# Optimization experiments

Measured on AMD Instinct MI355X. Metric: run time of the kernel, lower is better.

Reference implementation:

```python
import jax, jax.numpy as jnp
import numpy as np


def _block_triu_mask(seq_len, rows_per_block, cols_per_block, dtype=jnp.float32):
    # Block upper-triangular mask: block (i, j) is ones iff j >= i.
    tri = jnp.triu(jnp.ones((seq_len, seq_len), dtype=dtype))
    return jnp.kron(tri, jnp.ones((rows_per_block, cols_per_block), dtype=dtype))


def setup_inputs() -> dict:
    key = jax.random.key(0)
    k_x, k_w1, k_w2 = jax.random.split(key, 3)
    seq_len, input_dim, hidden_dim, output_dim = 64, 64, 128, 64
    batch = 256
    x = jax.random.normal(k_x, (batch, seq_len, input_dim), dtype=jnp.float32)
    # kaiming_uniform_(a=sqrt(5)) on [fan_in, fan_out] tensor -> bound = 1/sqrt(fan_in)
    fan1 = seq_len * input_dim
    W1 = jax.random.uniform(k_w1, (seq_len * input_dim, seq_len * hidden_dim),
                            minval=-1.0, maxval=1.0, dtype=jnp.float32) / np.sqrt(fan1)
    b1 = jnp.zeros((seq_len * hidden_dim,), dtype=jnp.float32)
    fan2 = seq_len * hidden_dim
    W2 = jax.random.uniform(k_w2, (seq_len * hidden_dim, seq_len * output_dim),
                            minval=-1.0, maxval=1.0, dtype=jnp.float32) / np.sqrt(fan2)
    b2 = jnp.zeros((seq_len * output_dim,), dtype=jnp.float32)
    return {"x": x, "W1": W1, "b1": b1, "W2": W2, "b2": b2, "seq_len": seq_len}


def reference(x, W1, b1, W2, b2, seq_len):
    batch = x.shape[0]
    input_dim = x.shape[2]
    hidden_dim = W1.shape[1] // seq_len
    output_dim = W2.shape[1] // seq_len
    mask1 = _block_triu_mask(seq_len, input_dim, hidden_dim, W1.dtype)
    mask2 = _block_triu_mask(seq_len, hidden_dim, output_dim, W2.dtype)
    h = x.reshape(batch, seq_len * input_dim)
    h = jnp.matmul(h, W1 * mask1) + b1           # [B, S*H]
    h = jax.nn.relu(h)
    h = jnp.matmul(h, W2 * mask2) + b2           # [B, S*O]
    return h.reshape(batch, seq_len, output_dim)
```

## Files before the change

kernel.cpp:

```cpp
#include <hip/hip_runtime.h>

typedef short bf16x8 __attribute__((ext_vector_type(8)));
typedef float f32x4 __attribute__((ext_vector_type(4)));

__device__ __forceinline__ unsigned short f2bf(float f) {
  unsigned x = __float_as_uint(f);
  return (unsigned short)((x + 0x7fffu + ((x >> 16) & 1u)) >> 16);
}


__device__ __forceinline__ int chunkbase1(int p) {
  const int a = p >> 1, b = p & 1;
  const int al = a >> 3, be = a & 7;
  const int C8 = 4 * al * (al + 1) + be * (al + 1);
  return 2 * C8 + b * ((a + 8) >> 3);
}
__device__ __forceinline__ int chunkbase2(int p) {
  const int al = p >> 2, be = p & 3;
  return 2 * al * (al + 1) + be * (al + 1);
}

__global__ __launch_bounds__(256)
void pack_x(const float* __restrict__ x, unsigned short* __restrict__ img) {
  const int i = (blockIdx.x * 256 + threadIdx.x) * 8;
  const int m = i >> 12, k = i & 4095;
  float q[8];
  *(float4*)(q)     = *(const float4*)(x + i);
  *(float4*)(q + 4) = *(const float4*)(x + i + 4);
  union { unsigned short u[8]; int4 v; } t;
#pragma unroll
  for (int j = 0; j < 8; ++j) t.u[j] = f2bf(q[j]);
  const size_t o = (size_t)(k >> 6) * 16384 + m * 64 + ((k & 63) ^ ((m & 7) << 3));
  *(int4*)(img + o) = t.v;
}

template<int PSH, int KSH, int MODE>
__global__ __launch_bounds__(256, 2)
void gemm_sk(const unsigned short* __restrict__ Aimg,
             const float* __restrict__ W,
             float* __restrict__ part, int N) {
  __shared__ unsigned short Ws[64 * 72];

  const int p = (int)gridDim.x - 1 - (int)blockIdx.x;
  const int c = blockIdx.y;
  const int nt = ((p >> PSH) + 1) << KSH;
  const int i0 = c * 8;
  if (i0 >= nt) return;
  const int i1 = (i0 + 8 < nt) ? i0 + 8 : nt;
  const int base = (MODE == 1) ? chunkbase1(p) : chunkbase2(p);
  float* po = part + (size_t)(base + c) * 16384;

  const int tid = threadIdx.x, lane = tid & 63, wave = tid >> 6;
  const int l15 = lane & 15, quad = lane >> 4;

  const int l16 = tid & 15, rg = tid >> 4;
  const float* wbase = W + (size_t)p * 64 + l16 * 4;

  int aoff[4][2];
#pragma unroll
  for (int mi = 0; mi < 4; ++mi) {
    const int m = wave * 64 + mi * 16 + l15;
#pragma unroll
    for (int h = 0; h < 2; ++h) {
      const int k8 = h * 32 + quad * 8;
      aoff[mi][h] = m * 64 + (k8 ^ ((m & 7) << 3));
    }
  }

  float4 wr[4];
  bf16x8 afA[4][2], afB[4][2];

  auto loadW = [&](int kt) {
#pragma unroll
    for (int j = 0; j < 4; ++j)
      wr[j] = *(const float4*)(wbase + (size_t)(kt * 64 + rg + j * 16) * N);
  };
  auto loadA = [&](bf16x8 (&af)[4][2], int kt) {
    const unsigned short* at = Aimg + (size_t)kt * 16384;
#pragma unroll
    for (int mi = 0; mi < 4; ++mi)
#pragma unroll
      for (int h = 0; h < 2; ++h)
        af[mi][h] = *(const bf16x8*)(at + aoff[mi][h]);
  };
  auto storeW = [&]() {
#pragma unroll
    for (int j = 0; j < 4; ++j) {
      const int r = rg + j * 16;
      const float* f = (const float*)&wr[j];
#pragma unroll
      for (int i = 0; i < 4; ++i) {
        const int cc = l16 * 4 + i;
        Ws[cc * 72 + (r ^ (((cc >> 3) & 7) << 3))] = f2bf(f[i]);
      }
    }
  };

  f32x4 acc[4][4];
#pragma unroll
  for (int mi = 0; mi < 4; ++mi)
#pragma unroll
    for (int ni = 0; ni < 4; ++ni)
      acc[mi][ni] = (f32x4){0.f, 0.f, 0.f, 0.f};

  auto STEP = [&](bf16x8 (&cur)[4][2], bf16x8 (&nxt)[4][2], int it) {
    __syncthreads();
    storeW();
    if (it + 1 < i1) { loadW(it + 1); loadA(nxt, it + 1); }
    __syncthreads();
#pragma unroll
    for (int h = 0; h < 2; ++h) {
      const int kk = h * 32;
      bf16x8 bfr[4];
#pragma unroll
      for (int ni = 0; ni < 4; ++ni) {
        const int n = ni * 16 + l15;
        bfr[ni] = *(const bf16x8*)(
            &Ws[n * 72 + ((kk + quad * 8) ^ (((n >> 3) & 7) << 3))]);
      }
#pragma unroll
      for (int mi = 0; mi < 4; ++mi)
#pragma unroll
        for (int ni = 0; ni < 4; ++ni)
          acc[mi][ni] = __builtin_amdgcn_mfma_f32_16x16x32_bf16(
              cur[mi][h], bfr[ni], acc[mi][ni], 0, 0, 0);
    }
  };

  loadW(i0);
  loadA(afA, i0);
  int it = i0;
  while (true) {
    STEP(afA, afB, it); if (++it >= i1) break;
    STEP(afB, afA, it); if (++it >= i1) break;
  }

  float* ps = po + wave * 4096 + lane;
#pragma unroll
  for (int mi = 0; mi < 4; ++mi)
#pragma unroll
    for (int ni = 0; ni < 4; ++ni)
#pragma unroll
      for (int r = 0; r < 4; ++r)
        ps[mi * 1024 + ni * 256 + r * 64] = acc[mi][ni][r];
}

__global__ __launch_bounds__(256)
void reduce1(const float* __restrict__ P, const float* __restrict__ b1,
             unsigned short* __restrict__ img) {
  const int g = blockIdx.x * 256 + threadIdx.x;
  const int p = g >> 12;
  const int s = (g & 4095) * 4;
  const int nc = ((p >> 1) + 8) >> 3;
  const float* ps = P + (size_t)chunkbase1(p) * 16384 + s;
  f32x4 a = *(const f32x4*)ps;
  for (int ci = 1; ci < nc; ++ci)
    a += *(const f32x4*)(ps + (size_t)ci * 16384);
  const int lane = s & 63, r = (s >> 6) & 3, ni = (s >> 8) & 3;
  const int mi = (s >> 10) & 3, wv = (s >> 12) & 3;
  const int m  = wv * 64 + mi * 16 + (lane >> 4) * 4 + r;
  const int nl = ni * 16 + (lane & 15);
  a += *(const f32x4*)(b1 + p * 64 + nl);
  union { unsigned short u[4]; int2 v; } t;
#pragma unroll
  for (int j = 0; j < 4; ++j) t.u[j] = f2bf(fmaxf(a[j], 0.f));
  *(int2*)(img + (size_t)p * 16384 + m * 64 + (nl ^ ((m & 7) << 3))) = t.v;
}

__global__ __launch_bounds__(256)
void reduce2(const float* __restrict__ P, const float* __restrict__ b2,
             float* __restrict__ out) {
  const int g = blockIdx.x * 256 + threadIdx.x;
  const int p = g >> 12;
  const int s = (g & 4095) * 4;
  const int nc = (p + 4) >> 2;
  const float* ps = P + (size_t)chunkbase2(p) * 16384 + s;
  f32x4 a = *(const f32x4*)ps;
  for (int ci = 1; ci < nc; ++ci)
    a += *(const f32x4*)(ps + (size_t)ci * 16384);
  const int lane = s & 63, r = (s >> 6) & 3, ni = (s >> 8) & 3;
  const int mi = (s >> 10) & 3, wv = (s >> 12) & 3;
  const int m  = wv * 64 + mi * 16 + (lane >> 4) * 4 + r;
  const int nl = ni * 16 + (lane & 15);
  a += *(const f32x4*)(b2 + p * 64 + nl);
  *(f32x4*)(out + (size_t)m * 4096 + p * 64 + nl) = a;
}

extern "C" void kernel_launch(void* const* d_in, const int* in_sizes, int n_in,
                              void* d_out, int out_size, void* d_ws, size_t ws_size,
                              hipStream_t stream) {
  const float* x  = (const float*)d_in[0];
  const float* W1 = (const float*)d_in[1];
  const float* b1 = (const float*)d_in[2];
  const float* W2 = (const float*)d_in[3];
  const float* b2 = (const float*)d_in[4];

  char* ws = (char*)d_ws;
  unsigned short* Ximg = (unsigned short*)ws;
  unsigned short* Himg = (unsigned short*)(ws + 2097152);
  float*          P    = (float*)(ws + 6291456);
  float* out = (float*)d_out;

  pack_x<<<dim3(512), 256, 0, stream>>>(x, Ximg);

  gemm_sk<1, 0, 1><<<dim3(128, 8), 256, 0, stream>>>(Ximg, W1, P, 8192);

  reduce1<<<dim3(2048), 256, 0, stream>>>(P, b1, Himg);

  gemm_sk<0, 1, 2><<<dim3(64, 16), 256, 0, stream>>>(Himg, W2, P, 4096);

  reduce2<<<dim3(1024), 256, 0, stream>>>(P, b2, out);
}
```

Measured before the change: 338.5 us.

## Widen GEMM tiles to 128x256 with LDS-staged A and fused x packing

Replaces the 256x64-tile split-K GEMM with a 512-thread kernel that computes 128x256 tiles, stages both A and W through shared memory, and converts x from fp32 to bf16 inside the GEMM so the separate pack kernel disappears. Panels now span 256 output columns, with per-element masking applied at the partial diagonal block. The goal is more reuse of each W load across output rows and fewer launches. The cost is that some masked-out W is still loaded, a larger LDS footprint, and a new partial-sum layout that the reductions must follow.

```diff
diff --git a/kernel.cpp b/kernel.cpp
--- a/kernel.cpp
+++ b/kernel.cpp
@@ -7,92 +7,96 @@
   unsigned x = __float_as_uint(f);
   return (unsigned short)((x + 0x7fffu + ((x >> 16) & 1u)) >> 16);
 }
-
-
-__device__ __forceinline__ int chunkbase1(int p) {
-  const int a = p >> 1, b = p & 1;
-  const int al = a >> 3, be = a & 7;
-  const int C8 = 4 * al * (al + 1) + be * (al + 1);
-  return 2 * C8 + b * ((a + 8) >> 3);
-}
-__device__ __forceinline__ int chunkbase2(int p) {
-  const int al = p >> 2, be = p & 3;
-  return 2 * al * (al + 1) + be * (al + 1);
-}
-
-__global__ __launch_bounds__(256)
-void pack_x(const float* __restrict__ x, unsigned short* __restrict__ img) {
-  const int i = (blockIdx.x * 256 + threadIdx.x) * 8;
-  const int m = i >> 12, k = i & 4095;
-  float q[8];
-  *(float4*)(q)     = *(const float4*)(x + i);
-  *(float4*)(q + 4) = *(const float4*)(x + i + 4);
-  union { unsigned short u[8]; int4 v; } t;
-#pragma unroll
-  for (int j = 0; j < 8; ++j) t.u[j] = f2bf(q[j]);
-  const size_t o = (size_t)(k >> 6) * 16384 + m * 64 + ((k & 63) ^ ((m & 7) << 3));
-  *(int4*)(img + o) = t.v;
-}
-
-template<int PSH, int KSH, int MODE>
-__global__ __launch_bounds__(256, 2)
-void gemm_sk(const unsigned short* __restrict__ Aimg,
-             const float* __restrict__ W,
-             float* __restrict__ part, int N) {
-  __shared__ unsigned short Ws[64 * 72];
-
-  const int p = (int)gridDim.x - 1 - (int)blockIdx.x;
-  const int c = blockIdx.y;
-  const int nt = ((p >> PSH) + 1) << KSH;
+__device__ __forceinline__ unsigned b32pair(float a, float b) {
+  return (unsigned)f2bf(a) | ((unsigned)f2bf(b) << 16);
+}
+
+template<int MODE>
+__global__ __launch_bounds__(512, 2)
+void gemm_w(const void* __restrict__ Av, const float* __restrict__ W,
+            float* __restrict__ P) {
+  constexpr int NPAN = (MODE == 1) ? 32 : 16;
+  constexpr int K    = (MODE == 1) ? 4096 : 8192;
+  constexpr int N    = (MODE == 1) ? 8192 : 4096;
+
+  __shared__ unsigned short Ws[256 * 64];
+  __shared__ unsigned short Xs[128 * 64];
+
+  const int p  = NPAN - 1 - (int)blockIdx.z;
+  const int mt = blockIdx.y;
+  const int c  = blockIdx.x;
+  const int nt = (MODE == 1) ? (2 * p + 2) : (8 * p + 8);
   const int i0 = c * 8;
   if (i0 >= nt) return;
-  const int i1 = (i0 + 8 < nt) ? i0 + 8 : nt;
-  const int base = (MODE == 1) ? chunkbase1(p) : chunkbase2(p);
-  float* po = part + (size_t)(base + c) * 16384;
-
-  const int tid = threadIdx.x, lane = tid & 63, wave = tid >> 6;
+  const int i1 = (i0 + 8 < nt) ? (i0 + 8) : nt;
+  const int a4 = p >> 2;
+  const int base = (MODE == 1) ? ((a4 + 1) * (2 * a4 + (p & 3)))
+                               : (p * (p + 1) / 2);
+  float* po = P + ((size_t)(base + c) * 2 + mt) * 32768;
+
+  const int tid = threadIdx.x;
+  const int lane = tid & 63, w = tid >> 6;
   const int l15 = lane & 15, quad = lane >> 4;
-
-  const int l16 = tid & 15, rg = tid >> 4;
-  const float* wbase = W + (size_t)p * 64 + l16 * 4;
-
-  int aoff[4][2];
-#pragma unroll
-  for (int mi = 0; mi < 4; ++mi) {
-    const int m = wave * 64 + mi * 16 + l15;
-#pragma unroll
-    for (int h = 0; h < 2; ++h) {
-      const int k8 = h * 32 + quad * 8;
-      aoff[mi][h] = m * 64 + (k8 ^ ((m & 7) << 3));
-    }
-  }
-
-  float4 wr[4];
-  bf16x8 afA[4][2], afB[4][2];
+  const int wm = w >> 2, wn = w & 3;
+  const int swa = (l15 & 7) << 3;
+
+  const int wr0 = (tid >> 4) * 2;
+  const int wc0 = (tid & 15) * 16;
+  const float* wsrc = W + (size_t)p * 256 + wc0;
+
+  const int ar = tid >> 2;
+  const int ak0 = (tid & 3) * 16;
+
+  float4 wv[8];
+  float4 av[4];
+  int4   ab[2];
 
   auto loadW = [&](int kt) {
-#pragma unroll
-    for (int j = 0; j < 4; ++j)
-      wr[j] = *(const float4*)(wbase + (size_t)(kt * 64 + rg + j * 16) * N);
-  };
-  auto loadA = [&](bf16x8 (&af)[4][2], int kt) {
-    const unsigned short* at = Aimg + (size_t)kt * 16384;
-#pragma unroll
-    for (int mi = 0; mi < 4; ++mi)
-#pragma unroll
-      for (int h = 0; h < 2; ++h)
-        af[mi][h] = *(const bf16x8*)(at + aoff[mi][h]);
-  };
-  auto storeW = [&]() {
-#pragma unroll
-    for (int j = 0; j < 4; ++j) {
-      const int r = rg + j * 16;
-      const float* f = (const float*)&wr[j];
-#pragma unroll
-      for (int i = 0; i < 4; ++i) {
-        const int cc = l16 * 4 + i;
-        Ws[cc * 72 + (r ^ (((cc >> 3) & 7) << 3))] = f2bf(f[i]);
+    const float* r0p = wsrc + (size_t)(kt * 64 + wr0) * N;
+#pragma unroll
+    for (int j = 0; j < 4; ++j) wv[j] = *(const float4*)(r0p + j * 4);
+#pragma unroll
+    for (int j = 0; j < 4; ++j) wv[4 + j] = *(const float4*)(r0p + N + j * 4);
+  };
+  auto storeW = [&](int kt) {
+    const int kg = kt * 64 + wr0;
+    const float* f = (const float*)wv;
+#pragma unroll
+    for (int i = 0; i < 16; ++i) {
+      const int cc = wc0 + i;
+      const int lk = (MODE == 1) ? ((2 * p + (cc >> 7) + 1) * 64)
+                                 : ((4 * p + (cc >> 6) + 1) * 128);
+      const float v0 = (kg < lk) ? f[i] : 0.f;
+      const float v1 = (kg + 1 < lk) ? f[16 + i] : 0.f;
+      const int sw = ((cc ^ (cc >> 3)) & 7) << 3;
+      *(unsigned*)&Ws[cc * 64 + (wr0 ^ sw)] = b32pair(v0, v1);
+    }
+  };
+  auto loadA = [&](int kt) {
+    if constexpr (MODE == 1) {
+      const float* ap = (const float*)Av + (size_t)(mt * 128 + ar) * K
+                        + kt * 64 + ak0;
+#pragma unroll
+      for (int j = 0; j < 4; ++j) av[j] = *(const float4*)(ap + j * 4);
+    } else {
+      const unsigned short* ap = (const unsigned short*)Av
+          + (size_t)(mt * 128 + ar) * K + kt * 64 + ak0;
+      ab[0] = *(const int4*)ap;
+      ab[1] = *(const int4*)(ap + 8);
+    }
+  };
+  auto storeA = [&]() {
+    if constexpr (MODE == 1) {
+      const float* f = (const float*)av;
+      const int sa = (ar & 7) << 3;
+#pragma unroll
+      for (int j = 0; j < 8; ++j) {
+        const int kl = ak0 + 2 * j;
+        *(unsigned*)&Xs[ar * 64 + (kl ^ sa)] = b32pair(f[2 * j], f[2 * j + 1]);
       }
+    } else {
+      *(int4*)&Xs[ar * 64 + ak0]     = ab[0];
+      *(int4*)&Xs[ar * 64 + ak0 + 8] = ab[1];
     }
   };
 
@@ -103,87 +107,86 @@
     for (int ni = 0; ni < 4; ++ni)
       acc[mi][ni] = (f32x4){0.f, 0.f, 0.f, 0.f};
 
-  auto STEP = [&](bf16x8 (&cur)[4][2], bf16x8 (&nxt)[4][2], int it) {
+  loadW(i0);
+  loadA(i0);
+  for (int it = i0; it < i1; ++it) {
     __syncthreads();
-    storeW();
-    if (it + 1 < i1) { loadW(it + 1); loadA(nxt, it + 1); }
+    storeW(it);
+    storeA();
+    if (it + 1 < i1) { loadW(it + 1); loadA(it + 1); }
     __syncthreads();
 #pragma unroll
-    for (int h = 0; h < 2; ++h) {
-      const int kk = h * 32;
-      bf16x8 bfr[4];
+    for (int kk = 0; kk < 64; kk += 32) {
+      bf16x8 af[4], bfr[4];
+#pragma unroll
+      for (int mi = 0; mi < 4; ++mi)
+        af[mi] = *(const bf16x8*)&Xs[(wm * 64 + mi * 16 + l15) * 64
+                                     + ((kk + quad * 8) ^ swa)];
 #pragma unroll
       for (int ni = 0; ni < 4; ++ni) {
-        const int n = ni * 16 + l15;
-        bfr[ni] = *(const bf16x8*)(
-            &Ws[n * 72 + ((kk + quad * 8) ^ (((n >> 3) & 7) << 3))]);
+        const int cc = wn * 64 + ni * 16 + l15;
+        const int sw = ((cc ^ (cc >> 3)) & 7) << 3;
+        bfr[ni] = *(const bf16x8*)&Ws[cc * 64 + ((kk + quad * 8) ^ sw)];
       }
 #pragma unroll
       for (int mi = 0; mi < 4; ++mi)
 #pragma unroll
         for (int ni = 0; ni < 4; ++ni)
           acc[mi][ni] = __builtin_amdgcn_mfma_f32_16x16x32_bf16(
-              cur[mi][h], bfr[ni], acc[mi][ni], 0, 0, 0);
-    }
-  };
-
-  loadW(i0);
-  loadA(afA, i0);
-  int it = i0;
-  while (true) {
-    STEP(afA, afB, it); if (++it >= i1) break;
-    STEP(afB, afA, it); if (++it >= i1) break;
+              af[mi], bfr[ni], acc[mi][ni], 0, 0, 0);
+    }
   }
 
-  float* ps = po + wave * 4096 + lane;
+  float* ps = po + w * 4096 + lane;
 #pragma unroll
   for (int mi = 0; mi < 4; ++mi)
 #pragma unroll
     for (int ni = 0; ni < 4; ++ni)
 #pragma unroll
       for (int r = 0; r < 4; ++r)
-        ps[mi * 1024 + ni * 256 + r * 64] = acc[mi][ni][r];
+        ps[ni * 64 + r * 256 + mi * 1024] = acc[mi][ni][r];
 }
 
 __global__ __launch_bounds__(256)
 void reduce1(const float* __restrict__ P, const float* __restrict__ b1,
-             unsigned short* __restrict__ img) {
+             unsigned short* __restrict__ Hs) {
   const int g = blockIdx.x * 256 + threadIdx.x;
-  const int p = g >> 12;
-  const int s = (g & 4095) * 4;
-  const int nc = ((p >> 1) + 8) >> 3;
-  const float* ps = P + (size_t)chunkbase1(p) * 16384 + s;
+  const int m = g >> 11, n0 = (g & 2047) * 4;
+  const int p = n0 >> 8, nl = n0 & 255, ml = m & 127, mb = m >> 7;
+  const int a4 = p >> 2;
+  const int base = (a4 + 1) * (2 * a4 + (p & 3));
+  const int nc = a4 + 1;
+  const int lane = ((ml >> 2) & 3) * 16 + (nl & 15);
+  const int s = lane + ((nl >> 4) & 3) * 64 + (ml & 3) * 256
+              + ((ml >> 4) & 3) * 1024 + (((ml >> 6) << 2) + (nl >> 6)) * 4096;
+  const float* ps = P + ((size_t)base * 2 + mb) * 32768 + s;
   f32x4 a = *(const f32x4*)ps;
   for (int ci = 1; ci < nc; ++ci)
-    a += *(const f32x4*)(ps + (size_t)ci * 16384);
-  const int lane = s & 63, r = (s >> 6) & 3, ni = (s >> 8) & 3;
-  const int mi = (s >> 10) & 3, wv = (s >> 12) & 3;
-  const int m  = wv * 64 + mi * 16 + (lane >> 4) * 4 + r;
-  const int nl = ni * 16 + (lane & 15);
-  a += *(const f32x4*)(b1 + p * 64 + nl);
+    a += *(const f32x4*)(ps + (size_t)ci * 65536);
+  a += *(const f32x4*)(b1 + n0);
   union { unsigned short u[4]; int2 v; } t;
 #pragma unroll
   for (int j = 0; j < 4; ++j) t.u[j] = f2bf(fmaxf(a[j], 0.f));
-  *(int2*)(img + (size_t)p * 16384 + m * 64 + (nl ^ ((m & 7) << 3))) = t.v;
+  *(int2*)(Hs + (size_t)m * 8192 + (n0 ^ ((m & 7) << 3))) = t.v;
 }
 
 __global__ __launch_bounds__(256)
 void reduce2(const float* __restrict__ P, const float* __restrict__ b2,
              float* __restrict__ out) {
   const int g = blockIdx.x * 256 + threadIdx.x;
-  const int p = g >> 12;
-  const int s = (g & 4095) * 4;
-  const int nc = (p + 4) >> 2;
-  const float* ps = P + (size_t)chunkbase2(p) * 16384 + s;
+  const int m = g >> 10, n0 = (g & 1023) * 4;
+  const int p = n0 >> 8, nl = n0 & 255, ml = m & 127, mb = m >> 7;
+  const int base = p * (p + 1) / 2;
+  const int nc = p + 1;
+  const int lane = ((ml >> 2) & 3) * 16 + (nl & 15);
+  const int s = lane + ((nl >> 4) & 3) * 64 + (ml & 3) * 256
+              + ((ml >> 4) & 3) * 1024 + (((ml >> 6) << 2) + (nl >> 6)) * 4096;
+  const float* ps = P + ((size_t)base * 2 + mb) * 32768 + s;
   f32x4 a = *(const f32x4*)ps;
   for (int ci = 1; ci < nc; ++ci)
-    a += *(const f32x4*)(ps + (size_t)ci * 16384);
-  const int lane = s & 63, r = (s >> 6) & 3, ni = (s >> 8) & 3;
-  const int mi = (s >> 10) & 3, wv = (s >> 12) & 3;
-  const int m  = wv * 64 + mi * 16 + (lane >> 4) * 4 + r;
-  const int nl = ni * 16 + (lane & 15);
-  a += *(const f32x4*)(b2 + p * 64 + nl);
-  *(f32x4*)(out + (size_t)m * 4096 + p * 64 + nl) = a;
+    a += *(const f32x4*)(ps + (size_t)ci * 65536);
+  a += *(const f32x4*)(b2 + n0);
+  *(f32x4*)(out + (size_t)m * 4096 + n0) = a;
 }
 
 extern "C" void kernel_launch(void* const* d_in, const int* in_sizes, int n_in,
@@ -196,18 +199,15 @@
   const float* b2 = (const float*)d_in[4];
 
   char* ws = (char*)d_ws;
-  unsigned short* Ximg = (unsigned short*)ws;
-  unsigned short* Himg = (unsigned short*)(ws + 2097152);
-  float*          P    = (float*)(ws + 6291456);
+  unsigned short* Hs = (unsigned short*)ws;
+  float*          P  = (float*)(ws + 4194304);
   float* out = (float*)d_out;
 
-  pack_x<<<dim3(512), 256, 0, stream>>>(x, Ximg);
-
-  gemm_sk<1, 0, 1><<<dim3(128, 8), 256, 0, stream>>>(Ximg, W1, P, 8192);
-
-  reduce1<<<dim3(2048), 256, 0, stream>>>(P, b1, Himg);
-
-  gemm_sk<0, 1, 2><<<dim3(64, 16), 256, 0, stream>>>(Himg, W2, P, 4096);
+  gemm_w<1><<<dim3(8, 2, 32), 512, 0, stream>>>(x, W1, P);
+
+  reduce1<<<dim3(2048), 256, 0, stream>>>(P, b1, Hs);
+
+  gemm_w<2><<<dim3(16, 2, 16), 512, 0, stream>>>(Hs, W2, P);
 
   reduce2<<<dim3(1024), 256, 0, stream>>>(P, b2, out);
 }
```

New measurement: 372.9 us. +10.2%, slower.

## Retile split-K GEMMs to 128x128 tiles with double-buffered LDS weights

Applied to the files above, without the earlier changes.

Both block-triangular GEMMs move from 256x64 output tiles to 128x128 tiles, with a 2x2 wave layout and the M dimension split across the grid. Weight tiles are now double-buffered in shared memory, so each k-step needs one barrier instead of two and the next tile's loads overlap the current MFMAs. Packed activations use a row-major swizzled layout, and the reduce kernels and chunk indexing are rewritten to match. In the second GEMM, 128-wide panels straddle the triangle boundary, so partial tiles are zero-masked, which costs some extra MFMA work on masked-out weights.

```diff
diff --git a/kernel.cpp b/kernel.cpp
--- a/kernel.cpp
+++ b/kernel.cpp
@@ -7,18 +7,19 @@
   unsigned x = __float_as_uint(f);
   return (unsigned short)((x + 0x7fffu + ((x >> 16) & 1u)) >> 16);
 }
-
-
-__device__ __forceinline__ int chunkbase1(int p) {
+__device__ __forceinline__ unsigned b32pair(float a, float b) {
+  return (unsigned)f2bf(a) | ((unsigned)f2bf(b) << 16);
+}
+
+__device__ __forceinline__ int cbase1(int p) {
+  const int a = p >> 3, b = p & 7;
+  return (a + 1) * (4 * a + b);
+}
+__device__ __forceinline__ int cbase2(int p) {
   const int a = p >> 1, b = p & 1;
-  const int al = a >> 3, be = a & 7;
-  const int C8 = 4 * al * (al + 1) + be * (al + 1);
-  return 2 * C8 + b * ((a + 8) >> 3);
-}
-__device__ __forceinline__ int chunkbase2(int p) {
-  const int al = p >> 2, be = p & 3;
-  return 2 * al * (al + 1) + be * (al + 1);
-}
+  return (a + 1) * (a + b);
+}
+
 
 __global__ __launch_bounds__(256)
 void pack_x(const float* __restrict__ x, unsigned short* __restrict__ img) {
@@ -30,71 +31,75 @@
   union { unsigned short u[8]; int4 v; } t;
 #pragma unroll
   for (int j = 0; j < 8; ++j) t.u[j] = f2bf(q[j]);
-  const size_t o = (size_t)(k >> 6) * 16384 + m * 64 + ((k & 63) ^ ((m & 7) << 3));
-  *(int4*)(img + o) = t.v;
-}
-
-template<int PSH, int KSH, int MODE>
+  *(int4*)(img + (size_t)m * 4096 + (k ^ ((m & 7) << 3))) = t.v;
+}
+
+template<int MODE>
 __global__ __launch_bounds__(256, 2)
-void gemm_sk(const unsigned short* __restrict__ Aimg,
-             const float* __restrict__ W,
-             float* __restrict__ part, int N) {
-  __shared__ unsigned short Ws[64 * 72];
-
-  const int p = (int)gridDim.x - 1 - (int)blockIdx.x;
-  const int c = blockIdx.y;
-  const int nt = ((p >> PSH) + 1) << KSH;
+void gemm_w(const unsigned short* __restrict__ A, const float* __restrict__ W,
+            float* __restrict__ P) {
+  constexpr int NPAN = (MODE == 1) ? 64 : 32;
+  constexpr int AK   = (MODE == 1) ? 4096 : 8192;
+  constexpr int N    = (MODE == 1) ? 8192 : 4096;
+
+  __shared__ unsigned short Ws[2][128 * 64];
+
+  const int p  = NPAN - 1 - (int)blockIdx.z;
+  const int mt = blockIdx.y;
+  const int c  = blockIdx.x;
+  const int nt = (MODE == 1) ? (p + 1) : (4 * p + 4);
   const int i0 = c * 8;
   if (i0 >= nt) return;
-  const int i1 = (i0 + 8 < nt) ? i0 + 8 : nt;
-  const int base = (MODE == 1) ? chunkbase1(p) : chunkbase2(p);
-  float* po = part + (size_t)(base + c) * 16384;
-
-  const int tid = threadIdx.x, lane = tid & 63, wave = tid >> 6;
+  const int i1 = (i0 + 8 < nt) ? (i0 + 8) : nt;
+  const int bs = (MODE == 1) ? cbase1(p) : cbase2(p);
+  float* po = P + ((size_t)(bs + c) * 2 + mt) * 16384;
+
+  const int tid = threadIdx.x, lane = tid & 63, w = tid >> 6;
   const int l15 = lane & 15, quad = lane >> 4;
-
-  const int l16 = tid & 15, rg = tid >> 4;
-  const float* wbase = W + (size_t)p * 64 + l16 * 4;
+  const int wm = w >> 1, wn = w & 1;
+
+  const int wr0 = (tid >> 3) * 2;
+  const int wc0 = (tid & 7) * 16;
+  const float* wsrc = W + (size_t)p * 128 + wc0;
+  const int lk = (MODE == 2) ? (2 * p + 1 + (wc0 >> 6)) * 128 : 0x7fffffff;
 
   int aoff[4][2];
 #pragma unroll
   for (int mi = 0; mi < 4; ++mi) {
-    const int m = wave * 64 + mi * 16 + l15;
-#pragma unroll
-    for (int h = 0; h < 2; ++h) {
-      const int k8 = h * 32 + quad * 8;
-      aoff[mi][h] = m * 64 + (k8 ^ ((m & 7) << 3));
+    const int m = mt * 128 + wm * 64 + mi * 16 + l15;
+#pragma unroll
+    for (int h = 0; h < 2; ++h)
+      aoff[mi][h] = m * AK + ((h * 32 + quad * 8) ^ ((m & 7) << 3));
+  }
+
+  float4 wv[8];
+  auto loadW = [&](int kt) {
+    const float* r0 = wsrc + (size_t)(kt * 64 + wr0) * N;
+#pragma unroll
+    for (int j = 0; j < 4; ++j) wv[j] = *(const float4*)(r0 + j * 4);
+#pragma unroll
+    for (int j = 0; j < 4; ++j) wv[4 + j] = *(const float4*)(r0 + N + j * 4);
+  };
+  auto storeW = [&](int buf, int kt) {
+    const float* f = (const float*)wv;
+    const int kg = kt * 64 + wr0;
+#pragma unroll
+    for (int i = 0; i < 16; ++i) {
+      const int cc = wc0 + i;
+      float v0 = f[i], v1 = f[16 + i];
+      if (MODE == 2) { v0 = (kg < lk) ? v0 : 0.f; v1 = (kg + 1 < lk) ? v1 : 0.f; }
+      const int sw = ((cc ^ (cc >> 3)) & 7) << 3;
+      *(unsigned*)&Ws[buf][cc * 64 + (wr0 ^ sw)] = b32pair(v0, v1);
     }
-  }
-
-  float4 wr[4];
-  bf16x8 afA[4][2], afB[4][2];
-
-  auto loadW = [&](int kt) {
-#pragma unroll
-    for (int j = 0; j < 4; ++j)
-      wr[j] = *(const float4*)(wbase + (size_t)(kt * 64 + rg + j * 16) * N);
   };
   auto loadA = [&](bf16x8 (&af)[4][2], int kt) {
-    const unsigned short* at = Aimg + (size_t)kt * 16384;
+    const unsigned short* at = A + (size_t)kt * 64;
 #pragma unroll
     for (int mi = 0; mi < 4; ++mi)
 #pragma unroll
       for (int h = 0; h < 2; ++h)
         af[mi][h] = *(const bf16x8*)(at + aoff[mi][h]);
   };
-  auto storeW = [&]() {
-#pragma unroll
-    for (int j = 0; j < 4; ++j) {
-      const int r = rg + j * 16;
-      const float* f = (const float*)&wr[j];
-#pragma unroll
-      for (int i = 0; i < 4; ++i) {
-        const int cc = l16 * 4 + i;
-        Ws[cc * 72 + (r ^ (((cc >> 3) & 7) << 3))] = f2bf(f[i]);
-      }
-    }
-  };
 
   f32x4 acc[4][4];
 #pragma unroll
@@ -103,87 +108,95 @@
     for (int ni = 0; ni < 4; ++ni)
       acc[mi][ni] = (f32x4){0.f, 0.f, 0.f, 0.f};
 
-  auto STEP = [&](bf16x8 (&cur)[4][2], bf16x8 (&nxt)[4][2], int it) {
-    __syncthreads();
-    storeW();
-    if (it + 1 < i1) { loadW(it + 1); loadA(nxt, it + 1); }
-    __syncthreads();
+  bf16x8 afA[4][2], afB[4][2];
+
+  loadW(i0);
+  loadA(afA, i0);
+  storeW(0, i0);
+  __syncthreads();
+
+  int cur = 0;
+  auto ITER = [&](bf16x8 (&caf)[4][2], bf16x8 (&naf)[4][2], int t) {
+    const bool pre = (t + 1 < i1);
+    if (pre) { loadW(t + 1); loadA(naf, t + 1); }
+    const unsigned short* Wb = &Ws[cur][0];
 #pragma unroll
     for (int h = 0; h < 2; ++h) {
       const int kk = h * 32;
       bf16x8 bfr[4];
 #pragma unroll
       for (int ni = 0; ni < 4; ++ni) {
-        const int n = ni * 16 + l15;
-        bfr[ni] = *(const bf16x8*)(
-            &Ws[n * 72 + ((kk + quad * 8) ^ (((n >> 3) & 7) << 3))]);
+        const int cc = wn * 64 + ni * 16 + l15;
+        const int sw = ((cc ^ (cc >> 3)) & 7) << 3;
+        bfr[ni] = *(const bf16x8*)&Wb[cc * 64 + ((kk + quad * 8) ^ sw)];
       }
 #pragma unroll
       for (int mi = 0; mi < 4; ++mi)
 #pragma unroll
         for (int ni = 0; ni < 4; ++ni)
           acc[mi][ni] = __builtin_amdgcn_mfma_f32_16x16x32_bf16(
-              cur[mi][h], bfr[ni], acc[mi][ni], 0, 0, 0);
+              caf[mi][h], bfr[ni], acc[mi][ni], 0, 0, 0);
     }
-  };
-
-  loadW(i0);
-  loadA(afA, i0);
-  int it = i0;
+    if (pre) {
+      storeW(cur ^ 1, t + 1);
+      __syncthreads();
+    }
+    cur ^= 1;
+  };
+
+  int t = i0;
   while (true) {
-    STEP(afA, afB, it); if (++it >= i1) break;
-    STEP(afB, afA, it); if (++it >= i1) break;
+    ITER(afA, afB, t); if (++t >= i1) break;
+    ITER(afB, afA, t); if (++t >= i1) break;
   }
 
-  float* ps = po + wave * 4096 + lane;
+  float* ps = po + w * 4096 + lane;
 #pragma unroll
   for (int mi = 0; mi < 4; ++mi)
 #pragma unroll
     for (int ni = 0; ni < 4; ++ni)
 #pragma unroll
       for (int r = 0; r < 4; ++r)
-        ps[mi * 1024 + ni * 256 + r * 64] = acc[mi][ni][r];
+        ps[ni * 64 + r * 256 + mi * 1024] = acc[mi][ni][r];
 }
 
 __global__ __launch_bounds__(256)
 void reduce1(const float* __restrict__ P, const float* __restrict__ b1,
-             unsigned short* __restrict__ img) {
+             unsigned short* __restrict__ Hs) {
   const int g = blockIdx.x * 256 + threadIdx.x;
-  const int p = g >> 12;
-  const int s = (g & 4095) * 4;
-  const int nc = ((p >> 1) + 8) >> 3;
-  const float* ps = P + (size_t)chunkbase1(p) * 16384 + s;
+  const int m = g >> 11, n0 = (g & 2047) * 4;
+  const int p = n0 >> 7, nl = n0 & 127, mb = m >> 7, ml = m & 127;
+  const int s = (((ml >> 2) & 3) * 16 + (nl & 15)) + ((nl >> 4) & 3) * 64
+              + (ml & 3) * 256 + ((ml >> 4) & 3) * 1024
+              + (((ml >> 6) << 1) + (nl >> 6)) * 4096;
+  const int nc = (p + 8) >> 3;
+  const float* ps = P + ((size_t)cbase1(p) * 2 + mb) * 16384 + s;
   f32x4 a = *(const f32x4*)ps;
   for (int ci = 1; ci < nc; ++ci)
-    a += *(const f32x4*)(ps + (size_t)ci * 16384);
-  const int lane = s & 63, r = (s >> 6) & 3, ni = (s >> 8) & 3;
-  const int mi = (s >> 10) & 3, wv = (s >> 12) & 3;
-  const int m  = wv * 64 + mi * 16 + (lane >> 4) * 4 + r;
-  const int nl = ni * 16 + (lane & 15);
-  a += *(const f32x4*)(b1 + p * 64 + nl);
+    a += *(const f32x4*)(ps + (size_t)ci * 32768);
+  a += *(const f32x4*)(b1 + n0);
   union { unsigned short u[4]; int2 v; } t;
 #pragma unroll
   for (int j = 0; j < 4; ++j) t.u[j] = f2bf(fmaxf(a[j], 0.f));
-  *(int2*)(img + (size_t)p * 16384 + m * 64 + (nl ^ ((m & 7) << 3))) = t.v;
+  *(int2*)(Hs + (size_t)m * 8192 + (n0 ^ ((m & 7) << 3))) = t.v;
 }
 
 __global__ __launch_bounds__(256)
 void reduce2(const float* __restrict__ P, const float* __restrict__ b2,
              float* __restrict__ out) {
   const int g = blockIdx.x * 256 + threadIdx.x;
-  const int p = g >> 12;
-  const int s = (g & 4095) * 4;
-  const int nc = (p + 4) >> 2;
-  const float* ps = P + (size_t)chunkbase2(p) * 16384 + s;
+  const int m = g >> 10, n0 = (g & 1023) * 4;
+  const int p = n0 >> 7, nl = n0 & 127, mb = m >> 7, ml = m & 127;
+  const int s = (((ml >> 2) & 3) * 16 + (nl & 15)) + ((nl >> 4) & 3) * 64
+              + (ml & 3) * 256 + ((ml >> 4) & 3) * 1024
+              + (((ml >> 6) << 1) + (nl >> 6)) * 4096;
+  const int nc = (p + 2) >> 1;
+  const float* ps = P + ((size_t)cbase2(p) * 2 + mb) * 16384 + s;
   f32x4 a = *(const f32x4*)ps;
   for (int ci = 1; ci < nc; ++ci)
-    a += *(const f32x4*)(ps + (size_t)ci * 16384);
-  const int lane = s & 63, r = (s >> 6) & 3, ni = (s >> 8) & 3;
-  const int mi = (s >> 10) & 3, wv = (s >> 12) & 3;
-  const int m  = wv * 64 + mi * 16 + (lane >> 4) * 4 + r;
-  const int nl = ni * 16 + (lane & 15);
-  a += *(const f32x4*)(b2 + p * 64 + nl);
-  *(f32x4*)(out + (size_t)m * 4096 + p * 64 + nl) = a;
+    a += *(const f32x4*)(ps + (size_t)ci * 32768);
+  a += *(const f32x4*)(b2 + n0);
+  *(f32x4*)(out + (size_t)m * 4096 + n0) = a;
 }
 
 extern "C" void kernel_launch(void* const* d_in, const int* in_sizes, int n_in,
@@ -197,17 +210,17 @@
 
   char* ws = (char*)d_ws;
   unsigned short* Ximg = (unsigned short*)ws;
-  unsigned short* Himg = (unsigned short*)(ws + 2097152);
+  unsigned short* Hs   = (unsigned short*)(ws + 2097152);
   float*          P    = (float*)(ws + 6291456);
   float* out = (float*)d_out;
 
   pack_x<<<dim3(512), 256, 0, stream>>>(x, Ximg);
 
-  gemm_sk<1, 0, 1><<<dim3(128, 8), 256, 0, stream>>>(Ximg, W1, P, 8192);
-
-  reduce1<<<dim3(2048), 256, 0, stream>>>(P, b1, Himg);
-
-  gemm_sk<0, 1, 2><<<dim3(64, 16), 256, 0, stream>>>(Himg, W2, P, 4096);
+  gemm_w<1><<<dim3(8, 2, 64), 256, 0, stream>>>(Ximg, W1, P);
+
+  reduce1<<<dim3(2048), 256, 0, stream>>>(P, b1, Hs);
+
+  gemm_w<2><<<dim3(16, 2, 32), 256, 0, stream>>>(Hs, W2, P);
 
   reduce2<<<dim3(1024), 256, 0, stream>>>(P, b2, out);
 }
```

Result: slower. 354.7 us (+4.8%).
